# Kernel optimization log

Hardware: AMD Instinct MI355X
Metric: run time of the kernel (lower is better)

## Reference

```python
import jax, jax.numpy as jnp
import numpy as np

EMB = 256
HID = 512
VOCAB = 32000
SRC_LEN = 50
TRG_LEN = 50
BATCH = 64


def lstm_layer(x, h0, c0, Wih, Whh, b):
    """x: [T,B,in]; h0,c0: [B,H]; Wih: [4H,in]; Whh: [4H,H]; b: [4H].
    PyTorch gate order i,f,g,o. Returns (ys [T,B,H], hT, cT)."""
    def step(carry, xt):
        h, c = carry
        g = xt @ Wih.T + h @ Whh.T + b
        i, f, gg, o = jnp.split(g, 4, axis=-1)
        c = jax.nn.sigmoid(f) * c + jax.nn.sigmoid(i) * jnp.tanh(gg)
        h = jax.nn.sigmoid(o) * jnp.tanh(c)
        return (h, c), h
    (hT, cT), ys = jax.lax.scan(step, (h0, c0), x)
    return ys, hT, cT


def setup_inputs() -> dict:
    key = jax.random.key(0)
    ks = jax.random.split(key, 20)
    s = 0.05
    d = {
        'src': jax.random.randint(ks[0], (SRC_LEN, BATCH), 0, VOCAB),
        'trg': jax.random.randint(ks[1], (TRG_LEN, BATCH), 0, VOCAB),
        'enc_emb': jax.random.normal(ks[2], (VOCAB, EMB), jnp.float32) * s,
        'enc_Wih0': jax.random.normal(ks[3], (4 * HID, EMB), jnp.float32) * s,
        'enc_Whh0': jax.random.normal(ks[4], (4 * HID, HID), jnp.float32) * s,
        'enc_b0': jnp.zeros((4 * HID,), jnp.float32),
        'enc_Wih1': jax.random.normal(ks[5], (4 * HID, HID), jnp.float32) * s,
        'enc_Whh1': jax.random.normal(ks[6], (4 * HID, HID), jnp.float32) * s,
        'enc_b1': jnp.zeros((4 * HID,), jnp.float32),
        'dec_emb': jax.random.normal(ks[7], (VOCAB, EMB), jnp.float32) * s,
        'dec_Wih0': jax.random.normal(ks[8], (4 * HID, EMB), jnp.float32) * s,
        'dec_Whh0': jax.random.normal(ks[9], (4 * HID, HID), jnp.float32) * s,
        'dec_b0': jnp.zeros((4 * HID,), jnp.float32),
        'dec_Wih1': jax.random.normal(ks[10], (4 * HID, HID), jnp.float32) * s,
        'dec_Whh1': jax.random.normal(ks[11], (4 * HID, HID), jnp.float32) * s,
        'dec_b1': jnp.zeros((4 * HID,), jnp.float32),
        'out_W': jax.random.normal(ks[12], (VOCAB, HID), jnp.float32) * s,
        'out_b': jnp.zeros((VOCAB,), jnp.float32),
    }
    return d


def reference(src, trg, enc_emb, enc_Wih0, enc_Whh0, enc_b0, enc_Wih1, enc_Whh1,
              enc_b1, dec_emb, dec_Wih0, dec_Whh0, dec_b0, dec_Wih1, dec_Whh1,
              dec_b1, out_W, out_b):
    B = src.shape[1]
    z = jnp.zeros((B, HID), enc_emb.dtype)
    # Encoder: 2-layer LSTM over src, keep final (h, c) per layer
    xe = enc_emb[src]                                   # [S,B,E]
    y0, h0, c0 = lstm_layer(xe, z, z, enc_Wih0, enc_Whh0, enc_b0)
    _, h1, c1 = lstm_layer(y0, z, z, enc_Wih1, enc_Whh1, enc_b1)
    # Decoder with teacher forcing: inputs are trg[0:T-1]
    xd = dec_emb[trg[:-1]]                              # [T-1,B,E]
    d0, _, _ = lstm_layer(xd, h0, c0, dec_Wih0, dec_Whh0, dec_b0)
    d1, _, _ = lstm_layer(d0, h1, c1, dec_Wih1, dec_Whh1, dec_b1)
    preds = d1 @ out_W.T + out_b                        # [T-1,B,V]
    return preds
```

## Files before the change

### kernel.cpp

```cpp
#include <hip/hip_runtime.h>
#include <hip/hip_bf16.h>

#define BATCH 64
#define HID 512
#define EMB 256
#define VOCAB 32000
#define G4 2048

typedef __attribute__((ext_vector_type(8))) short short8;
typedef __attribute__((ext_vector_type(4))) float f32x4;
typedef __attribute__((ext_vector_type(4))) unsigned short ush4;

__global__ __launch_bounds__(256) void zero_kernel(float* p, int n){
    int i = blockIdx.x*256 + threadIdx.x;
    if (i < n) p[i] = 0.f;
}

__device__ __forceinline__ unsigned short bf16_rne(float x){
    unsigned b = __float_as_uint(x);
    return (unsigned short)((b + 0x7fffu + ((b >> 16) & 1u)) >> 16);
}
__device__ __forceinline__ void split2(float x, unsigned short& h, unsigned short& l){
    h = bf16_rne(x);
    l = bf16_rne(x - __uint_as_float((unsigned)h << 16));
}

__global__ __launch_bounds__(256) void embed_kernel(const int* __restrict__ tok,
                                                    const float* __restrict__ emb,
                                                    float* __restrict__ out, int T){
    int i = blockIdx.x*256 + threadIdx.x;
    int n = T*BATCH*(EMB/4);
    if (i >= n) return;
    int e4 = i % (EMB/4);
    int tb = i / (EMB/4);
    int id = tok[tb];
    reinterpret_cast<float4*>(out)[(size_t)tb*(EMB/4) + e4] =
        reinterpret_cast<const float4*>(emb + (size_t)id*EMB)[e4];
}

__global__ __launch_bounds__(256) void embed_plane_kernel(const int* __restrict__ tok,
                                                          const float* __restrict__ emb,
                                                          unsigned short* __restrict__ hi,
                                                          unsigned short* __restrict__ lo, int T){
    int i = blockIdx.x*256 + threadIdx.x;
    int n = T*BATCH*(EMB/4);
    if (i >= n) return;
    int e4 = i % (EMB/4);
    int tb = i / (EMB/4);
    int id = tok[tb];
    f32x4 v = reinterpret_cast<const f32x4*>(emb + (size_t)id*EMB)[e4];
    ush4 h, l;
    #pragma unroll
    for (int j = 0; j < 4; j++){ unsigned short a,b; split2(v[j], a, b); h[j]=a; l[j]=b; }
    reinterpret_cast<ush4*>(hi)[(size_t)tb*(EMB/4) + e4] = h;
    reinterpret_cast<ush4*>(lo)[(size_t)tb*(EMB/4) + e4] = l;
}

__global__ __launch_bounds__(256) void split_kernel(const float* __restrict__ in,
                                                    unsigned short* __restrict__ hi,
                                                    unsigned short* __restrict__ lo, int n4){
    int i = blockIdx.x*256 + threadIdx.x;
    if (i >= n4) return;
    f32x4 v = reinterpret_cast<const f32x4*>(in)[i];
    ush4 h, l;
    #pragma unroll
    for (int j = 0; j < 4; j++){ unsigned short a,b; split2(v[j], a, b); h[j]=a; l[j]=b; }
    reinterpret_cast<ush4*>(hi)[i] = h;
    reinterpret_cast<ush4*>(lo)[i] = l;
}

__global__ __launch_bounds__(256) void split_hi_kernel(const float* __restrict__ in,
                                                       unsigned short* __restrict__ hi, int n4){
    int i = blockIdx.x*256 + threadIdx.x;
    if (i >= n4) return;
    f32x4 v = reinterpret_cast<const f32x4*>(in)[i];
    ush4 h;
    #pragma unroll
    for (int j = 0; j < 4; j++) h[j] = bf16_rne(v[j]);
    reinterpret_cast<ush4*>(hi)[i] = h;
}

template<int KDIM, int NDIM>
__global__ __launch_bounds__(256) void gemm_mfma_split(
    const float* __restrict__ A, const float* __restrict__ B,
    const float* __restrict__ bias, float* __restrict__ C, int M)
{
    constexpr int LS = 40;
    __shared__ unsigned short Ah[128*LS], Al[128*LS], Bh[128*LS], Bl[128*LS];
    const int n0 = blockIdx.x*128, m0 = blockIdx.y*128;
    const int tid  = threadIdx.x;
    const int lane = tid & 63, wid = tid >> 6;
    const int wm = wid >> 1, wn = wid & 1;
    const int srow = tid >> 1, sk = (tid & 1)*16;
    f32x4 acc[4][4] = {};

    for (int k0 = 0; k0 < KDIM; k0 += 32){
        __syncthreads();
        {
            int ar = m0 + srow;
            float xv[16];
            if (ar < M){
                const float4* ap = reinterpret_cast<const float4*>(A + (size_t)ar*KDIM + k0 + sk);
                #pragma unroll
                for (int q = 0; q < 4; q++){
                    float4 v = ap[q];
                    xv[q*4+0]=v.x; xv[q*4+1]=v.y; xv[q*4+2]=v.z; xv[q*4+3]=v.w;
                }
            } else {
                #pragma unroll
                for (int q = 0; q < 16; q++) xv[q] = 0.f;
            }
            #pragma unroll
            for (int q = 0; q < 16; q++){
                unsigned short h,l; split2(xv[q], h, l);
                Ah[srow*LS + sk + q] = h;
                Al[srow*LS + sk + q] = l;
            }
        }
        {
            int br = n0 + srow;
            const float4* bp = reinterpret_cast<const float4*>(B + (size_t)br*KDIM + k0 + sk);
            #pragma unroll
            for (int q = 0; q < 4; q++){
                float4 v = bp[q];
                float xs[4] = {v.x, v.y, v.z, v.w};
                #pragma unroll
                for (int j = 0; j < 4; j++){
                    unsigned short h,l; split2(xs[j], h, l);
                    Bh[srow*LS + sk + q*4 + j] = h;
                    Bl[srow*LS + sk + q*4 + j] = l;
                }
            }
        }
        __syncthreads();
        const int fr = lane & 15, fk = (lane >> 4)*8;
        short8 a_h[4], a_l[4], b_h[4], b_l[4];
        #pragma unroll
        for (int mi = 0; mi < 4; mi++){
            int row = wm*64 + mi*16 + fr;
            a_h[mi] = *reinterpret_cast<const short8*>(&Ah[row*LS + fk]);
            a_l[mi] = *reinterpret_cast<const short8*>(&Al[row*LS + fk]);
        }
        #pragma unroll
        for (int nj = 0; nj < 4; nj++){
            int rowb = wn*64 + nj*16 + fr;
            b_h[nj] = *reinterpret_cast<const short8*>(&Bh[rowb*LS + fk]);
            b_l[nj] = *reinterpret_cast<const short8*>(&Bl[rowb*LS + fk]);
        }
        #pragma unroll
        for (int mi = 0; mi < 4; mi++)
            #pragma unroll
            for (int nj = 0; nj < 4; nj++){
                acc[mi][nj] = __builtin_amdgcn_mfma_f32_16x16x32_bf16(a_h[mi], b_h[nj], acc[mi][nj], 0,0,0);
                acc[mi][nj] = __builtin_amdgcn_mfma_f32_16x16x32_bf16(a_h[mi], b_l[nj], acc[mi][nj], 0,0,0);
                acc[mi][nj] = __builtin_amdgcn_mfma_f32_16x16x32_bf16(a_l[mi], b_h[nj], acc[mi][nj], 0,0,0);
            }
    }
    const int fr = lane & 15, fq = lane >> 4;
    #pragma unroll
    for (int nj = 0; nj < 4; nj++){
        int col = n0 + wn*64 + nj*16 + fr;
        float bv = bias[col];
        #pragma unroll
        for (int mi = 0; mi < 4; mi++){
            int rbase = m0 + wm*64 + mi*16 + fq*4;
            #pragma unroll
            for (int j = 0; j < 4; j++){
                int row = rbase + j;
                if (row < M)
                    __builtin_nontemporal_store(acc[mi][nj][j] + bv, &C[(size_t)row*NDIM + col]);
            }
        }
    }
}

__device__ __forceinline__ void gll16(const unsigned short* g, unsigned short* l){
    __builtin_amdgcn_global_load_lds(
        (const __attribute__((address_space(1))) unsigned int*)g,
        (__attribute__((address_space(3))) unsigned int*)l, 16, 0, 0);
}

template<int KDIM, int NDIM, int NTN, int PASSES>
__global__ __launch_bounds__(256) void gemm_planes_gll(
    const unsigned short* __restrict__ Ahi, const unsigned short* __restrict__ Alo,
    const unsigned short* __restrict__ Bhi, const unsigned short* __restrict__ Blo,
    const float* __restrict__ bias, float* __restrict__ C, int M)
{
    constexpr int NP = (PASSES == 3) ? 4 : 2;
    __shared__ unsigned short P[NP][128*32];
    const int total = gridDim.x;
    const int q = total >> 3, r8 = total & 7;
    const int xcd = blockIdx.x & 7, idx = blockIdx.x >> 3;
    const int lid = (xcd < r8 ? xcd*(q+1) : r8*(q+1) + (xcd - r8)*q) + idx;
    const int m0 = (lid / NTN)*128, n0 = (lid % NTN)*128;

    const int tid  = threadIdx.x;
    const int lane = tid & 63, wid = tid >> 6;
    const int wm = wid >> 1, wn = wid & 1;

    const unsigned short* gsrc;
    int row0;
    bool stager;
    if (PASSES == 3){
        gsrc = (wid == 0) ? Ahi : (wid == 1) ? Alo : (wid == 2) ? Bhi : Blo;
        row0 = (wid < 2) ? m0 : n0;
        stager = true;
    } else {
        gsrc = (wid == 0) ? Ahi : Bhi;
        row0 = (wid == 0) ? m0 : n0;
        stager = (wid < 2);
    }
    const unsigned short* gbase = gsrc + (size_t)(row0 + (lane >> 2))*KDIM
                                       + 8*((lane & 3) ^ ((lane >> 3) & 3));
    unsigned short* lbase = &P[(wid < NP) ? wid : 0][0];

    f32x4 acc[4][4] = {};

    for (int k0 = 0; k0 < KDIM; k0 += 32){
        __syncthreads();
        if (stager){
            #pragma unroll
            for (int i = 0; i < 8; i++)
                gll16(gbase + k0 + (size_t)i*16*KDIM, lbase + i*512);
        }
        __syncthreads();

        const int fr = lane & 15, fkq = lane >> 4;
        const int swz = 8*(fkq ^ ((fr >> 1) & 3));
        constexpr int BHP = (PASSES == 3) ? 2 : 1;
        short8 a_h[4], a_l[4], b_h[4], b_l[4];
        #pragma unroll
        for (int mi = 0; mi < 4; mi++){
            int row = wm*64 + mi*16 + fr;
            a_h[mi] = *reinterpret_cast<const short8*>(&P[0][row*32 + swz]);
            if (PASSES == 3)
                a_l[mi] = *reinterpret_cast<const short8*>(&P[1][row*32 + swz]);
        }
        #pragma unroll
        for (int nj = 0; nj < 4; nj++){
            int row = wn*64 + nj*16 + fr;
            b_h[nj] = *reinterpret_cast<const short8*>(&P[BHP][row*32 + swz]);
            if (PASSES == 3)
                b_l[nj] = *reinterpret_cast<const short8*>(&P[3][row*32 + swz]);
        }
        #pragma unroll
        for (int mi = 0; mi < 4; mi++)
            #pragma unroll
            for (int nj = 0; nj < 4; nj++){
                acc[mi][nj] = __builtin_amdgcn_mfma_f32_16x16x32_bf16(a_h[mi], b_h[nj], acc[mi][nj], 0,0,0);
                if (PASSES == 3){
                    acc[mi][nj] = __builtin_amdgcn_mfma_f32_16x16x32_bf16(a_l[mi], b_h[nj], acc[mi][nj], 0,0,0);
                    acc[mi][nj] = __builtin_amdgcn_mfma_f32_16x16x32_bf16(a_h[mi], b_l[nj], acc[mi][nj], 0,0,0);
                }
            }
    }
    const int fr = lane & 15, fq = lane >> 4;
    #pragma unroll
    for (int nj = 0; nj < 4; nj++){
        int col = n0 + wn*64 + nj*16 + fr;
        float bv = bias[col];
        #pragma unroll
        for (int mi = 0; mi < 4; mi++){
            int rbase = m0 + wm*64 + mi*16 + fq*4;
            #pragma unroll
            for (int j = 0; j < 4; j++){
                int row = rbase + j;
                if (row < M)
                    __builtin_nontemporal_store(acc[mi][nj][j] + bv, &C[(size_t)row*NDIM + col]);
            }
        }
    }
}

__device__ __forceinline__ void lstm_body(
    const float* __restrict__ Xp, const float* __restrict__ Whh,
    const float* __restrict__ hinit, const float* __restrict__ cinit,
    float* __restrict__ ys, float* __restrict__ cfin,
    int T, unsigned* __restrict__ flagbase, int bx,
    unsigned short* __restrict__ phi, unsigned short* __restrict__ plo)
{
    constexpr int WS = 520;
    __shared__ unsigned short hH[8*WS], hL[8*WS];
    __shared__ float red[2048 + 128];
    __shared__ unsigned short zbuf[8];

    const int hc  = bx & 31, bc = bx >> 5;
    const int hid0 = hc*16;
    const int tid = threadIdx.x;
    const int lane = tid & 63, kc = tid >> 6;
    const int fr = lane & 15, fkq = lane >> 4;
    unsigned* myflag = flagbase + (size_t)(bc*32 + hc)*16;

    if (tid < 8) zbuf[tid] = 0;

    short8 ah[4][4], al[4][4];
    #pragma unroll
    for (int m = 0; m < 4; m++){
        const float* wr = Whh + (size_t)(m*HID + hid0 + fr)*HID;
        #pragma unroll
        for (int s = 0; s < 4; s++){
            int k0 = kc*128 + s*32 + fkq*8;
            f32x4 v0 = *reinterpret_cast<const f32x4*>(wr + k0);
            f32x4 v1 = *reinterpret_cast<const f32x4*>(wr + k0 + 4);
            short8 h8, l8;
            float xv[8] = {v0[0],v0[1],v0[2],v0[3],v1[0],v1[1],v1[2],v1[3]};
            #pragma unroll
            for (int j = 0; j < 8; j++){
                unsigned short hh, ll; split2(xv[j], hh, ll);
                h8[j] = (short)hh; l8[j] = (short)ll;
            }
            ah[m][s] = h8; al[m][s] = l8;
        }
    }

    const int ub = tid >> 4;
    const int uh = tid & 15;
    float creg = 0.f;
    if (tid < 128) creg = cinit[(size_t)(bc*8 + ub)*HID + hid0 + uh];

    const size_t hbase = (size_t)bc*8*HID;
    const float* xprow = Xp + (size_t)(bc*8 + ub)*G4 + hid0 + uh;

    float xn0=0.f, xn1=0.f, xn2=0.f, xn3=0.f;
    if (tid < 128){
        const float* xpr = xprow;
        xn0 = xpr[0]; xn1 = xpr[512]; xn2 = xpr[1024]; xn3 = xpr[1536];
    }

    for (int t = 0; t < T; t++){
        {
            const f32x4* hsrc = reinterpret_cast<const f32x4*>(
                (t == 0) ? (hinit + hbase) : (ys + (size_t)(t-1)*BATCH*HID + hbase));
            #pragma unroll
            for (int j = 0; j < 4; j++){
                int fidx = tid + j*256;
                f32x4 v = hsrc[fidx];
                int e   = fidx*4;
                int row = e >> 9, col = e & 511;
                ush4 h, l;
                #pragma unroll
                for (int qq = 0; qq < 4; qq++){ unsigned short a,b; split2(v[qq], a, b); h[qq]=a; l[qq]=b; }
                *reinterpret_cast<ush4*>(&hH[row*WS + col]) = h;
                *reinterpret_cast<ush4*>(&hL[row*WS + col]) = l;
            }
        }
        __syncthreads();

        {
            f32x4 acc4[4] = {};
            const bool breal = fr < 8;
            #pragma unroll
            for (int s = 0; s < 4; s++){
                int k0 = kc*128 + s*32 + fkq*8;
                short8 bh = breal ? *reinterpret_cast<const short8*>(&hH[fr*WS + k0])
                                  : *reinterpret_cast<const short8*>(zbuf);
                short8 bl = breal ? *reinterpret_cast<const short8*>(&hL[fr*WS + k0])
                                  : *reinterpret_cast<const short8*>(zbuf);
                #pragma unroll
                for (int m = 0; m < 4; m++){
                    acc4[m] = __builtin_amdgcn_mfma_f32_16x16x32_bf16(ah[m][s], bh, acc4[m], 0,0,0);
                    acc4[m] = __builtin_amdgcn_mfma_f32_16x16x32_bf16(ah[m][s], bl, acc4[m], 0,0,0);
                    acc4[m] = __builtin_amdgcn_mfma_f32_16x16x32_bf16(al[m][s], bh, acc4[m], 0,0,0);
                }
            }
            const int b = lane & 15;
            if (b < 8){
                #pragma unroll
                for (int m = 0; m < 4; m++)
                    #pragma unroll
                    for (int qq = 0; qq < 4; qq++){
                        int rowp = m*16 + (lane >> 4)*4 + qq;
                        red[kc*512 + rowp*8 + b] = acc4[m][qq];
                    }
            }
        }
        __syncthreads();

        if (tid < 64){
            #pragma unroll
            for (int b = 0; b < 8; b++)
                red[tid*8 + b] = red[tid*8 + b] + red[512 + tid*8 + b]
                               + red[1024 + tid*8 + b] + red[1536 + tid*8 + b];
        }
        __syncthreads();

        if (tid < 128){
            float gi = red[(0*16 + uh)*8 + ub] + xn0;
            float gf = red[(1*16 + uh)*8 + ub] + xn1;
            float gg = red[(2*16 + uh)*8 + ub] + xn2;
            float go = red[(3*16 + uh)*8 + ub] + xn3;
            float si = 1.f/(1.f + expf(-gi));
            float sf = 1.f/(1.f + expf(-gf));
            float so = 1.f/(1.f + expf(-go));
            float tg = tanhf(gg);
            float c = sf*creg + si*tg;
            creg = c;
            float hval = so * tanhf(c);
            red[2048 + tid] = hval;
            if (phi){
                unsigned short hh, ll; split2(hval, hh, ll);
                size_t poff = (size_t)t*BATCH*HID + (size_t)(bc*8 + ub)*HID + hid0 + uh;
                phi[poff] = hh; plo[poff] = ll;
            }
            if (t < T-1){
                const float* xpr = xprow + (size_t)(t+1)*BATCH*G4;
                xn0 = xpr[0]; xn1 = xpr[512]; xn2 = xpr[1024]; xn3 = xpr[1536];
            }
        }
        __syncthreads();

        if (tid < 64){
            if (tid < 32){
                f32x4 v = *reinterpret_cast<const f32x4*>(&red[2048 + tid*4]);
                const f32x4* addr = reinterpret_cast<const f32x4*>(
                    ys + (size_t)t*BATCH*HID
                       + (size_t)(bc*8 + (tid >> 2))*HID + hid0 + (tid & 3)*4);
                asm volatile("global_store_dwordx4 %0, %1, off sc0 sc1"
                             :: "v"(addr), "v"(v) : "memory");
            }
            if (t < T-1){
                asm volatile("s_waitcnt vmcnt(0)" ::: "memory");
                if (tid == 0)
                    __hip_atomic_store(myflag, (unsigned)(t+1),
                                       __ATOMIC_RELAXED, __HIP_MEMORY_SCOPE_AGENT);
                const unsigned tgt = (unsigned)(t+1);
                unsigned* fp = flagbase + (size_t)(bc*32 + (tid & 31))*16;
                unsigned spins = 0;
                bool done = false;
                while (!done && spins < (1u<<20)){
                    unsigned v = tgt;
                    if (tid < 32)
                        v = __hip_atomic_load(fp, __ATOMIC_RELAXED, __HIP_MEMORY_SCOPE_AGENT);
                    done = (bool)__all((int)(v >= tgt));
                    spins++;
                }
            }
        }
        __syncthreads();
    }

    if (tid < 128)
        cfin[(size_t)(bc*8 + ub)*HID + hid0 + uh] = creg;
}

__global__ __launch_bounds__(256, 2) void lstm_layer_k(
    const float* Xp, const float* Whh, const float* hinit, const float* cinit,
    float* ys, float* cfin, int T, unsigned* flagbase,
    unsigned short* phi, unsigned short* plo)
{
    lstm_body(Xp, Whh, hinit, cinit, ys, cfin, T, flagbase, blockIdx.x, phi, plo);
}

__global__ __launch_bounds__(256, 2) void lstm_dual_k(
    const float* Xp0, const float* Whh0, const float* hi0, const float* ci0,
    float* ys0, float* cf0, int T0, unsigned* fl0,
    unsigned short* phi0, unsigned short* plo0,
    const float* Xp1, const float* Whh1, const float* hi1, const float* ci1,
    float* ys1, float* cf1, int T1, unsigned* fl1,
    unsigned short* phi1, unsigned short* plo1)
{
    const int role = blockIdx.x >> 8;
    const int bx = blockIdx.x & 255;
    if (role == 0)
        lstm_body(Xp0, Whh0, hi0, ci0, ys0, cf0, T0, fl0, bx, phi0, plo0);
    else
        lstm_body(Xp1, Whh1, hi1, ci1, ys1, cf1, T1, fl1, bx, phi1, plo1);
}

extern "C" void kernel_launch(void* const* d_in, const int* in_sizes, int n_in,
                              void* d_out, int out_size, void* d_ws, size_t ws_size,
                              hipStream_t stream) {
    const int*   src      = (const int*)  d_in[0];
    const int*   trg      = (const int*)  d_in[1];
    const float* enc_emb  = (const float*)d_in[2];
    const float* enc_Wih0 = (const float*)d_in[3];
    const float* enc_Whh0 = (const float*)d_in[4];
    const float* enc_b0   = (const float*)d_in[5];
    const float* enc_Wih1 = (const float*)d_in[6];
    const float* enc_Whh1 = (const float*)d_in[7];
    const float* enc_b1   = (const float*)d_in[8];
    const float* dec_emb  = (const float*)d_in[9];
    const float* dec_Wih0 = (const float*)d_in[10];
    const float* dec_Whh0 = (const float*)d_in[11];
    const float* dec_b0   = (const float*)d_in[12];
    const float* dec_Wih1 = (const float*)d_in[13];
    const float* dec_Whh1 = (const float*)d_in[14];
    const float* dec_b1   = (const float*)d_in[15];
    const float* out_W    = (const float*)d_in[16];
    const float* out_b    = (const float*)d_in[17];

    float* ob = (float*)d_out;
    float* Xp   = ob;
    float* xe   = ob + (size_t)6553600;
    float* xd   = ob + (size_t)7372800;
    float* eys0 = ob + (size_t)8175616;
    float* eys1 = ob + (size_t)9814016;
    float* dys0 = ob + (size_t)11452416;
    float* Xp2  = ob + (size_t)13058048;

    float* ws = (float*)d_ws;
    float* dys1 = ws;
    float* c0   = ws + (size_t)1605632;
    float* c1   = ws + (size_t)1638400;
    float* hz   = ws + (size_t)1671168;
    unsigned* flags = (unsigned*)(ws + (size_t)1703936);
    unsigned short* Whi = (unsigned short*)(ws + (size_t)1720320);
    unsigned short* Wlo = Whi + (size_t)16384000;
    unsigned short* Ahi = Wlo + (size_t)16384000;
    unsigned short* Alo = Ahi + (size_t)1638400;
    unsigned short* eW0h = Alo  + (size_t)1638400;
    unsigned short* eW0l = eW0h + (size_t)524288;
    unsigned short* eW1h = eW0l + (size_t)524288;
    unsigned short* eW1l = eW1h + (size_t)1048576;
    unsigned short* dW0h = eW1l + (size_t)1048576;
    unsigned short* dW0l = dW0h + (size_t)524288;
    unsigned short* dW1h = dW0l + (size_t)524288;
    unsigned short* dW1l = dW1h + (size_t)1048576;
    unsigned short* XAh  = dW1l + (size_t)1048576;
    unsigned short* XAl  = XAh  + (size_t)1638400;
    const size_t end_final = (size_t)1720320*4 + ((size_t)16384000 + 1638400)*2*2;
    const size_t end_xp    = end_final + ((size_t)6291456 + 3276800)*2;
    const bool xp_ok = (ws_size >= end_xp);

    {
        int n = 3*BATCH*HID + 4*4096;
        zero_kernel<<<(n+255)/256, 256, 0, stream>>>(c0, n);
    }

    if (xp_ok){
        split_hi_kernel<<<(16384000/4 + 255)/256, 256, 0, stream>>>(out_W, Whi, 16384000/4);
        split_kernel<<<(524288/4 + 255)/256, 256, 0, stream>>>(enc_Wih0, eW0h, eW0l, 524288/4);
        split_kernel<<<(1048576/4 + 255)/256, 256, 0, stream>>>(enc_Wih1, eW1h, eW1l, 1048576/4);
        split_kernel<<<(524288/4 + 255)/256, 256, 0, stream>>>(dec_Wih0, dW0h, dW0l, 524288/4);
        split_kernel<<<(1048576/4 + 255)/256, 256, 0, stream>>>(dec_Wih1, dW1h, dW1l, 1048576/4);
        embed_plane_kernel<<<(50*BATCH*(EMB/4)+255)/256, 256, 0, stream>>>(src, enc_emb, XAh, XAl, 50);
        embed_plane_kernel<<<(49*BATCH*(EMB/4)+255)/256, 256, 0, stream>>>(trg, dec_emb, Ahi, Alo, 49);
    } else {
        embed_kernel<<<(50*BATCH*(EMB/4)+255)/256, 256, 0, stream>>>(src, enc_emb, xe, 50);
        embed_kernel<<<(49*BATCH*(EMB/4)+255)/256, 256, 0, stream>>>(trg, dec_emb, xd, 49);
    }

    dim3 xgrid(G4/128, 25);

    if (xp_ok)
        gemm_planes_gll<EMB, G4, 16, 3><<<400, 256, 0, stream>>>(XAh, XAl, eW0h, eW0l, enc_b0, Xp, 3200);
    else
        gemm_mfma_split<EMB, G4><<<xgrid, 256, 0, stream>>>(xe, enc_Wih0, enc_b0, Xp, 3200);
    lstm_layer_k<<<256, 256, 0, stream>>>(Xp, enc_Whh0, hz, hz, eys0, c0, 50, flags + 0,
                                          xp_ok ? XAh : nullptr, XAl);

    if (xp_ok){
        gemm_planes_gll<HID, G4, 16, 3><<<400, 256, 0, stream>>>(XAh, XAl, eW1h, eW1l, enc_b1, Xp, 3200);
        gemm_planes_gll<EMB, G4, 16, 3><<<400, 256, 0, stream>>>(Ahi, Alo, dW0h, dW0l, dec_b0, Xp2, 3136);
    } else {
        gemm_mfma_split<HID, G4><<<xgrid, 256, 0, stream>>>(eys0, enc_Wih1, enc_b1, Xp, 3200);
        gemm_mfma_split<EMB, G4><<<xgrid, 256, 0, stream>>>(xd, dec_Wih0, dec_b0, Xp2, 3136);
    }

    lstm_dual_k<<<512, 256, 0, stream>>>(
        Xp,  enc_Whh1, hz,                          hz, eys1, c1, 50, flags + 4096,  nullptr, nullptr,
        Xp2, dec_Whh0, eys0 + (size_t)49*BATCH*HID, c0, dys0, c0, 49, flags + 8192,
        xp_ok ? XAh : nullptr, XAl);

    if (xp_ok)
        gemm_planes_gll<HID, G4, 16, 3><<<400, 256, 0, stream>>>(XAh, XAl, dW1h, dW1l, dec_b1, Xp, 3136);
    else
        gemm_mfma_split<HID, G4><<<xgrid, 256, 0, stream>>>(dys0, dec_Wih1, dec_b1, Xp, 3136);
    lstm_layer_k<<<256, 256, 0, stream>>>(Xp, dec_Whh1, eys1 + (size_t)49*BATCH*HID, c1,
                                          dys1, c1, 49, flags + 12288,
                                          xp_ok ? Ahi : nullptr, Alo);

    if (xp_ok){
        gemm_planes_gll<HID, VOCAB, 250, 1><<<6250, 256, 0, stream>>>(
            Ahi, Ahi, Whi, Whi, out_b, (float*)d_out, 3136);
    } else {
        gemm_mfma_split<HID, VOCAB><<<dim3(VOCAB/128, 25), 256, 0, stream>>>(
            dys1, out_W, out_b, (float*)d_out, 3136);
    }
}
```

Baseline: 952.9 us.

## Use 256x128 tiles for vocab projection GEMM and vectorize LSTM reduction stores

```diff
diff --git a/kernel.cpp b/kernel.cpp
--- a/kernel.cpp
+++ b/kernel.cpp
@@ -180,14 +180,13 @@
         (__attribute__((address_space(3))) unsigned int*)l, 16, 0, 0);
 }
 
-template<int KDIM, int NDIM, int NTN, int PASSES>
+template<int KDIM, int NDIM, int NTN>
 __global__ __launch_bounds__(256) void gemm_planes_gll(
     const unsigned short* __restrict__ Ahi, const unsigned short* __restrict__ Alo,
     const unsigned short* __restrict__ Bhi, const unsigned short* __restrict__ Blo,
     const float* __restrict__ bias, float* __restrict__ C, int M)
 {
-    constexpr int NP = (PASSES == 3) ? 4 : 2;
-    __shared__ unsigned short P[NP][128*32];
+    __shared__ unsigned short P[4][128*32];
     const int total = gridDim.x;
     const int q = total >> 3, r8 = total & 7;
     const int xcd = blockIdx.x & 7, idx = blockIdx.x >> 3;
@@ -198,60 +197,44 @@
     const int lane = tid & 63, wid = tid >> 6;
     const int wm = wid >> 1, wn = wid & 1;
 
-    const unsigned short* gsrc;
-    int row0;
-    bool stager;
-    if (PASSES == 3){
-        gsrc = (wid == 0) ? Ahi : (wid == 1) ? Alo : (wid == 2) ? Bhi : Blo;
-        row0 = (wid < 2) ? m0 : n0;
-        stager = true;
-    } else {
-        gsrc = (wid == 0) ? Ahi : Bhi;
-        row0 = (wid == 0) ? m0 : n0;
-        stager = (wid < 2);
-    }
+    const unsigned short* gsrc = (wid == 0) ? Ahi : (wid == 1) ? Alo
+                               : (wid == 2) ? Bhi : Blo;
+    const int row0 = (wid < 2) ? m0 : n0;
     const unsigned short* gbase = gsrc + (size_t)(row0 + (lane >> 2))*KDIM
                                        + 8*((lane & 3) ^ ((lane >> 3) & 3));
-    unsigned short* lbase = &P[(wid < NP) ? wid : 0][0];
+    unsigned short* lbase = &P[wid][0];
 
     f32x4 acc[4][4] = {};
 
     for (int k0 = 0; k0 < KDIM; k0 += 32){
         __syncthreads();
-        if (stager){
-            #pragma unroll
-            for (int i = 0; i < 8; i++)
-                gll16(gbase + k0 + (size_t)i*16*KDIM, lbase + i*512);
-        }
+        #pragma unroll
+        for (int i = 0; i < 8; i++)
+            gll16(gbase + k0 + (size_t)i*16*KDIM, lbase + i*512);
         __syncthreads();
 
         const int fr = lane & 15, fkq = lane >> 4;
         const int swz = 8*(fkq ^ ((fr >> 1) & 3));
-        constexpr int BHP = (PASSES == 3) ? 2 : 1;
         short8 a_h[4], a_l[4], b_h[4], b_l[4];
         #pragma unroll
         for (int mi = 0; mi < 4; mi++){
             int row = wm*64 + mi*16 + fr;
             a_h[mi] = *reinterpret_cast<const short8*>(&P[0][row*32 + swz]);
-            if (PASSES == 3)
-                a_l[mi] = *reinterpret_cast<const short8*>(&P[1][row*32 + swz]);
+            a_l[mi] = *reinterpret_cast<const short8*>(&P[1][row*32 + swz]);
         }
         #pragma unroll
         for (int nj = 0; nj < 4; nj++){
             int row = wn*64 + nj*16 + fr;
-            b_h[nj] = *reinterpret_cast<const short8*>(&P[BHP][row*32 + swz]);
-            if (PASSES == 3)
-                b_l[nj] = *reinterpret_cast<const short8*>(&P[3][row*32 + swz]);
+            b_h[nj] = *reinterpret_cast<const short8*>(&P[2][row*32 + swz]);
+            b_l[nj] = *reinterpret_cast<const short8*>(&P[3][row*32 + swz]);
         }
         #pragma unroll
         for (int mi = 0; mi < 4; mi++)
             #pragma unroll
             for (int nj = 0; nj < 4; nj++){
                 acc[mi][nj] = __builtin_amdgcn_mfma_f32_16x16x32_bf16(a_h[mi], b_h[nj], acc[mi][nj], 0,0,0);
-                if (PASSES == 3){
-                    acc[mi][nj] = __builtin_amdgcn_mfma_f32_16x16x32_bf16(a_l[mi], b_h[nj], acc[mi][nj], 0,0,0);
-                    acc[mi][nj] = __builtin_amdgcn_mfma_f32_16x16x32_bf16(a_h[mi], b_l[nj], acc[mi][nj], 0,0,0);
-                }
+                acc[mi][nj] = __builtin_amdgcn_mfma_f32_16x16x32_bf16(a_l[mi], b_h[nj], acc[mi][nj], 0,0,0);
+                acc[mi][nj] = __builtin_amdgcn_mfma_f32_16x16x32_bf16(a_h[mi], b_l[nj], acc[mi][nj], 0,0,0);
             }
     }
     const int fr = lane & 15, fq = lane >> 4;
@@ -262,6 +245,77 @@
         #pragma unroll
         for (int mi = 0; mi < 4; mi++){
             int rbase = m0 + wm*64 + mi*16 + fq*4;
+            #pragma unroll
+            for (int j = 0; j < 4; j++){
+                int row = rbase + j;
+                if (row < M)
+                    __builtin_nontemporal_store(acc[mi][nj][j] + bv, &C[(size_t)row*NDIM + col]);
+            }
+        }
+    }
+}
+
+template<int KDIM, int NDIM, int NTN>
+__global__ __launch_bounds__(256) void gemm_planes_256(
+    const unsigned short* __restrict__ Ahi,
+    const unsigned short* __restrict__ Bhi,
+    const float* __restrict__ bias, float* __restrict__ C, int M)
+{
+    __shared__ unsigned short Ah[256*32];
+    __shared__ unsigned short Bh[128*32];
+    const int total = gridDim.x;
+    const int q = total >> 3, r8 = total & 7;
+    const int xcd = blockIdx.x & 7, idx = blockIdx.x >> 3;
+    const int lid = (xcd < r8 ? xcd*(q+1) : r8*(q+1) + (xcd - r8)*q) + idx;
+    const int m0 = (lid / NTN)*256, n0 = (lid % NTN)*128;
+
+    const int tid  = threadIdx.x;
+    const int lane = tid & 63, wid = tid >> 6;
+    const int wm = wid >> 1, wn = wid & 1;
+
+    const unsigned short* gsrc = (wid < 2) ? Ahi : Bhi;
+    const int row0 = (wid == 0) ? m0 : (wid == 1) ? (m0 + 128) : n0;
+    const unsigned short* gbase = gsrc + (size_t)(row0 + (lane >> 2))*KDIM
+                                       + 8*((lane & 3) ^ ((lane >> 3) & 3));
+    unsigned short* lbase = (wid == 0) ? Ah : (wid == 1) ? (Ah + 128*32) : Bh;
+    const bool stager = (wid < 3);
+
+    f32x4 acc[8][4] = {};
+
+    for (int k0 = 0; k0 < KDIM; k0 += 32){
+        __syncthreads();
+        if (stager){
+            #pragma unroll
+            for (int i = 0; i < 8; i++)
+                gll16(gbase + k0 + (size_t)i*16*KDIM, lbase + i*512);
+        }
+        __syncthreads();
+
+        const int fr = lane & 15, fkq = lane >> 4;
+        const int swz = 8*(fkq ^ ((fr >> 1) & 3));
+        short8 b_h[4];
+        #pragma unroll
+        for (int nj = 0; nj < 4; nj++){
+            int row = wn*64 + nj*16 + fr;
+            b_h[nj] = *reinterpret_cast<const short8*>(&Bh[row*32 + swz]);
+        }
+        #pragma unroll
+        for (int mi = 0; mi < 8; mi++){
+            int row = wm*128 + mi*16 + fr;
+            short8 a = *reinterpret_cast<const short8*>(&Ah[row*32 + swz]);
+            #pragma unroll
+            for (int nj = 0; nj < 4; nj++)
+                acc[mi][nj] = __builtin_amdgcn_mfma_f32_16x16x32_bf16(a, b_h[nj], acc[mi][nj], 0,0,0);
+        }
+    }
+    const int fr = lane & 15, fq = lane >> 4;
+    #pragma unroll
+    for (int nj = 0; nj < 4; nj++){
+        int col = n0 + wn*64 + nj*16 + fr;
+        float bv = bias[col];
+        #pragma unroll
+        for (int mi = 0; mi < 8; mi++){
+            int rbase = m0 + wm*128 + mi*16 + fq*4;
             #pragma unroll
             for (int j = 0; j < 4; j++){
                 int row = rbase + j;
@@ -281,7 +335,7 @@
 {
     constexpr int WS = 520;
     __shared__ unsigned short hH[8*WS], hL[8*WS];
-    __shared__ float red[2048 + 128];
+    __shared__ __align__(16) float red[4*544 + 128];
     __shared__ unsigned short zbuf[8];
 
     const int hc  = bx & 31, bc = bx >> 5;
@@ -367,11 +421,7 @@
             if (b < 8){
                 #pragma unroll
                 for (int m = 0; m < 4; m++)
-                    #pragma unroll
-                    for (int qq = 0; qq < 4; qq++){
-                        int rowp = m*16 + (lane >> 4)*4 + qq;
-                        red[kc*512 + rowp*8 + b] = acc4[m][qq];
-                    }
+                    *reinterpret_cast<f32x4*>(&red[kc*544 + b*68 + m*16 + (lane >> 4)*4]) = acc4[m];
             }
         }
         __syncthreads();
@@ -379,16 +429,16 @@
         if (tid < 64){
             #pragma unroll
             for (int b = 0; b < 8; b++)
-                red[tid*8 + b] = red[tid*8 + b] + red[512 + tid*8 + b]
-                               + red[1024 + tid*8 + b] + red[1536 + tid*8 + b];
+                red[b*68 + tid] = red[b*68 + tid] + red[544 + b*68 + tid]
+                               + red[1088 + b*68 + tid] + red[1632 + b*68 + tid];
         }
         __syncthreads();
 
         if (tid < 128){
-            float gi = red[(0*16 + uh)*8 + ub] + xn0;
-            float gf = red[(1*16 + uh)*8 + ub] + xn1;
-            float gg = red[(2*16 + uh)*8 + ub] + xn2;
-            float go = red[(3*16 + uh)*8 + ub] + xn3;
+            float gi = red[ub*68 + 0*16 + uh] + xn0;
+            float gf = red[ub*68 + 1*16 + uh] + xn1;
+            float gg = red[ub*68 + 2*16 + uh] + xn2;
+            float go = red[ub*68 + 3*16 + uh] + xn3;
             float si = 1.f/(1.f + expf(-gi));
             float sf = 1.f/(1.f + expf(-gf));
             float so = 1.f/(1.f + expf(-go));
@@ -396,7 +446,7 @@
             float c = sf*creg + si*tg;
             creg = c;
             float hval = so * tanhf(c);
-            red[2048 + tid] = hval;
+            red[2176 + tid] = hval;
             if (phi){
                 unsigned short hh, ll; split2(hval, hh, ll);
                 size_t poff = (size_t)t*BATCH*HID + (size_t)(bc*8 + ub)*HID + hid0 + uh;
@@ -411,7 +461,7 @@
 
         if (tid < 64){
             if (tid < 32){
-                f32x4 v = *reinterpret_cast<const f32x4*>(&red[2048 + tid*4]);
+                f32x4 v = *reinterpret_cast<const f32x4*>(&red[2176 + tid*4]);
                 const f32x4* addr = reinterpret_cast<const f32x4*>(
                     ys + (size_t)t*BATCH*HID
                        + (size_t)(bc*8 + (tid >> 2))*HID + hid0 + (tid & 3)*4);
@@ -507,8 +557,8 @@
     unsigned short* Whi = (unsigned short*)(ws + (size_t)1720320);
     unsigned short* Wlo = Whi + (size_t)16384000;
     unsigned short* Ahi = Wlo + (size_t)16384000;
-    unsigned short* Alo = Ahi + (size_t)1638400;
-    unsigned short* eW0h = Alo  + (size_t)1638400;
+    unsigned short* Alo = Ahi + (size_t)1703936;
+    unsigned short* eW0h = Alo  + (size_t)1703936;
     unsigned short* eW0l = eW0h + (size_t)524288;
     unsigned short* eW1h = eW0l + (size_t)524288;
     unsigned short* eW1l = eW1h + (size_t)1048576;
@@ -518,8 +568,9 @@
     unsigned short* dW1l = dW1h + (size_t)1048576;
     unsigned short* XAh  = dW1l + (size_t)1048576;
     unsigned short* XAl  = XAh  + (size_t)1638400;
-    const size_t end_final = (size_t)1720320*4 + ((size_t)16384000 + 1638400)*2*2;
-    const size_t end_xp    = end_final + ((size_t)6291456 + 3276800)*2;
+    const size_t end_xp = (size_t)1720320*4 +
+        2*((size_t)16384000*2 + (size_t)1703936*2 + (size_t)524288*4 +
+           (size_t)1048576*4 + (size_t)1638400*2);
     const bool xp_ok = (ws_size >= end_xp);
 
     {
@@ -543,15 +594,15 @@
     dim3 xgrid(G4/128, 25);
 
     if (xp_ok)
-        gemm_planes_gll<EMB, G4, 16, 3><<<400, 256, 0, stream>>>(XAh, XAl, eW0h, eW0l, enc_b0, Xp, 3200);
+        gemm_planes_gll<EMB, G4, 16><<<400, 256, 0, stream>>>(XAh, XAl, eW0h, eW0l, enc_b0, Xp, 3200);
     else
         gemm_mfma_split<EMB, G4><<<xgrid, 256, 0, stream>>>(xe, enc_Wih0, enc_b0, Xp, 3200);
     lstm_layer_k<<<256, 256, 0, stream>>>(Xp, enc_Whh0, hz, hz, eys0, c0, 50, flags + 0,
                                           xp_ok ? XAh : nullptr, XAl);
 
     if (xp_ok){
-        gemm_planes_gll<HID, G4, 16, 3><<<400, 256, 0, stream>>>(XAh, XAl, eW1h, eW1l, enc_b1, Xp, 3200);
-        gemm_planes_gll<EMB, G4, 16, 3><<<400, 256, 0, stream>>>(Ahi, Alo, dW0h, dW0l, dec_b0, Xp2, 3136);
+        gemm_planes_gll<HID, G4, 16><<<400, 256, 0, stream>>>(XAh, XAl, eW1h, eW1l, enc_b1, Xp, 3200);
+        gemm_planes_gll<EMB, G4, 16><<<400, 256, 0, stream>>>(Ahi, Alo, dW0h, dW0l, dec_b0, Xp2, 3136);
     } else {
         gemm_mfma_split<HID, G4><<<xgrid, 256, 0, stream>>>(eys0, enc_Wih1, enc_b1, Xp, 3200);
         gemm_mfma_split<EMB, G4><<<xgrid, 256, 0, stream>>>(xd, dec_Wih0, dec_b0, Xp2, 3136);
@@ -563,7 +614,7 @@
         xp_ok ? XAh : nullptr, XAl);
 
     if (xp_ok)
-        gemm_planes_gll<HID, G4, 16, 3><<<400, 256, 0, stream>>>(XAh, XAl, dW1h, dW1l, dec_b1, Xp, 3136);
+        gemm_planes_gll<HID, G4, 16><<<400, 256, 0, stream>>>(XAh, XAl, dW1h, dW1l, dec_b1, Xp, 3136);
     else
         gemm_mfma_split<HID, G4><<<xgrid, 256, 0, stream>>>(dys0, dec_Wih1, dec_b1, Xp, 3136);
     lstm_layer_k<<<256, 256, 0, stream>>>(Xp, dec_Whh1, eys1 + (size_t)49*BATCH*HID, c1,
@@ -571,8 +622,8 @@
                                           xp_ok ? Ahi : nullptr, Alo);
 
     if (xp_ok){
-        gemm_planes_gll<HID, VOCAB, 250, 1><<<6250, 256, 0, stream>>>(
-            Ahi, Ahi, Whi, Whi, out_b, (float*)d_out, 3136);
+        gemm_planes_256<HID, VOCAB, 250><<<13*250, 256, 0, stream>>>(
+            Ahi, Whi, out_b, (float*)d_out, 3136);
     } else {
         gemm_mfma_split<HID, VOCAB><<<dim3(VOCAB/128, 25), 256, 0, stream>>>(
             dys1, out_W, out_b, (float*)d_out, 3136);
```

After: 1.136 ms. +19.2%, slower.
